# Performance work log

Hardware: AMD Instinct MI355X
Metric: run time of the kernel (lower is better)

## Reference

```python
import jax, jax.numpy as jnp
import numpy as np

N_NODES = 100000
N_EDGES = 1600000
IN_DIM, HID_DIM, OUT_DIM = 2, 128, 128


def setup_inputs() -> dict:
    key = jax.random.key(0)
    ks = jax.random.split(key, 8)
    x = jax.random.normal(ks[0], (N_NODES, IN_DIM), dtype=jnp.float32)
    edge_index = jax.random.randint(ks[1], (2, N_EDGES), 0, N_NODES, dtype=jnp.int64)
    s = 0.1
    return {
        "x": x,
        "edge_index": edge_index,
        # SAGEConv layer 1: lin_l (on aggregated neighbors, with bias) + lin_r (root)
        "W_l1": jax.random.normal(ks[2], (IN_DIM, HID_DIM), dtype=jnp.float32) * s,
        "W_r1": jax.random.normal(ks[3], (IN_DIM, HID_DIM), dtype=jnp.float32) * s,
        "b1": jnp.zeros((HID_DIM,), dtype=jnp.float32),
        # SAGEConv layer 2
        "W_l2": jax.random.normal(ks[4], (HID_DIM, OUT_DIM), dtype=jnp.float32) * s,
        "W_r2": jax.random.normal(ks[5], (HID_DIM, OUT_DIM), dtype=jnp.float32) * s,
        "b2": jnp.zeros((OUT_DIM,), dtype=jnp.float32),
    }


def _sage_conv(h, src, dst, Wl, Wr, b):
    # PyG SAGEConv (aggr='mean'): out_i = Wl @ mean_{j in N(i)} h_j + Wr @ h_i + b
    msg = h[src]                                              # [E, D] gather
    agg = jax.ops.segment_sum(msg, dst, num_segments=N_NODES)  # [N, D] scatter-add
    deg = jax.ops.segment_sum(jnp.ones_like(dst, dtype=h.dtype), dst,
                              num_segments=N_NODES)
    agg = agg / jnp.maximum(deg, 1.0)[:, None]                # mean aggregation
    return agg @ Wl + h @ Wr + b


def reference(x, edge_index, W_l1, W_r1, b1, W_l2, W_r2, b2):
    src, dst = edge_index[0], edge_index[1]  # messages flow src -> dst
    h = _sage_conv(x, src, dst, W_l1, W_r1, b1)
    h = jax.nn.relu(h)  # dropout p=0.1 is identity in eval mode
    out = _sage_conv(h, src, dst, W_l2, W_r2, b2)
    return out
```

## Files before the change

kernel.cpp:

```cpp
#include <hip/hip_runtime.h>


using f32x4 = __attribute__((ext_vector_type(4))) float;
using f32x2 = __attribute__((ext_vector_type(2))) float;
using s16x8 = __attribute__((ext_vector_type(8))) short;

__device__ __forceinline__ unsigned short f32_to_bf16(float f) {
  unsigned int u = __float_as_uint(f);
  u += 0x7fffu + ((u >> 16) & 1u);
  return (unsigned short)(u >> 16);
}

#define EDGE_TILE 4096

__global__ __launch_bounds__(256) void k_bhist(const int* __restrict__ ei, int* __restrict__ bcnt,
                                               unsigned short* __restrict__ hcnt, int E, int nb) {
  __shared__ int h[1024];
  int t = threadIdx.x;
  for (int i = t; i < nb; i += 256) h[i] = 0;
  __syncthreads();
  int tbeg = blockIdx.x * EDGE_TILE;
  int tend = min(tbeg + EDGE_TILE, E);
  const int* dstp = ei + E;
  for (int i = tbeg + t; i < tend; i += 256) atomicAdd(&h[dstp[i] >> 7], 1);
  __syncthreads();
  unsigned short* hr = hcnt + (size_t)blockIdx.x * nb;
  for (int i = t; i < nb; i += 256) {
    int c = h[i];
    hr[i] = (unsigned short)c;
    if (c) atomicAdd(&bcnt[i], c);
  }
}

__global__ __launch_bounds__(1024) void k_bscan(const int* __restrict__ bcnt, int* __restrict__ bbase,
                                                int nb, int E) {
  __shared__ int sm[2][1024];
  int t = threadIdx.x;
  int v0 = (t < nb) ? bcnt[t] : 0;
  sm[0][t] = v0;
  __syncthreads();
  int src = 0;
  for (int st = 1; st < 1024; st <<= 1) {
    int v = sm[src][t];
    if (t >= st) v += sm[src][t - st];
    sm[src ^ 1][t] = v; __syncthreads(); src ^= 1;
  }
  if (t < nb) bbase[t] = sm[src][t] - v0;
  if (t == 0) bbase[nb] = E;
}

__global__ __launch_bounds__(256) void k_colscan(const unsigned short* __restrict__ hcnt,
                                                 unsigned short* __restrict__ rel,
                                                 int nblk, int nb) {
  __shared__ int sm[2][256];
  int b = blockIdx.x;
  int t = threadIdx.x;
  int e0 = 2 * t, e1 = 2 * t + 1;
  int a = (e0 < nblk) ? (int)hcnt[(size_t)e0 * nb + b] : 0;
  int c = (e1 < nblk) ? (int)hcnt[(size_t)e1 * nb + b] : 0;
  int s = a + c;
  sm[0][t] = s;
  __syncthreads();
  int src = 0;
  for (int st = 1; st < 256; st <<= 1) {
    int v = sm[src][t];
    if (t >= st) v += sm[src][t - st];
    sm[src ^ 1][t] = v; __syncthreads(); src ^= 1;
  }
  int excl = sm[src][t] - s;
  if (e0 < nblk) rel[(size_t)e0 * nb + b] = (unsigned short)excl;
  if (e1 < nblk) rel[(size_t)e1 * nb + b] = (unsigned short)(excl + a);
}

__global__ __launch_bounds__(256) void k_bscatter(const int* __restrict__ ei,
                                                  const int* __restrict__ bbase,
                                                  const unsigned short* __restrict__ rel,
                                                  unsigned int* __restrict__ ebuf, int E, int nb) {
  __shared__ int h[1024];
  __shared__ int base[1024];
  int t = threadIdx.x;
  const unsigned short* rr = rel + (size_t)blockIdx.x * nb;
  for (int i = t; i < nb; i += 256) {
    h[i] = 0;
    base[i] = bbase[i] + (int)rr[i];
  }
  __syncthreads();
  int tbeg = blockIdx.x * EDGE_TILE;
  int tend = min(tbeg + EDGE_TILE, E);
  const int* srcp = ei;
  const int* dstp = ei + E;
  for (int i = tbeg + t; i < tend; i += 256) {
    int d = dstp[i];
    int b = d >> 7;
    int r = atomicAdd(&h[b], 1);
    ebuf[base[b] + r] = ((unsigned)srcp[i] << 7) | (unsigned)(d & 127);
  }
}

__global__ __launch_bounds__(256) void k_bucket_csr(const unsigned int* __restrict__ ebuf,
                                                    const int* __restrict__ bbase,
                                                    const float* __restrict__ x,
                                                    int* __restrict__ offs, int* __restrict__ csr,
                                                    float* __restrict__ agg1,
                                                    int N, int nb) {
  __shared__ int deg[128];
  __shared__ int loff[128];
  __shared__ int cur[128];
  __shared__ float sx0[128];
  __shared__ float sx1[128];
  int b = blockIdx.x;
  int t = threadIdx.x;
  int lo = bbase[b], hi = bbase[b + 1];
  if (t < 128) { deg[t] = 0; sx0[t] = 0.f; sx1[t] = 0.f; }
  __syncthreads();
  const float2* x2 = (const float2*)x;
  for (int i = lo + t; i < hi; i += 256) {
    unsigned int e = ebuf[i];
    int d = e & 127;
    float2 v = x2[e >> 7];
    atomicAdd(&deg[d], 1);
    atomicAdd(&sx0[d], v.x);
    atomicAdd(&sx1[d], v.y);
  }
  __syncthreads();
  if (t < 128) loff[t] = deg[t];
  __syncthreads();
  for (int st = 1; st < 128; st <<= 1) {
    int v = 0;
    if (t < 128 && t >= st) v = loff[t - st];
    __syncthreads();
    if (t < 128) loff[t] += v;
    __syncthreads();
  }
  if (t < 128) {
    int ex = loff[t] - deg[t];
    cur[t] = ex;
    int node = b * 128 + t;
    if (node < N) {
      offs[node] = lo + ex;
      agg1[2 * node]     = sx0[t];
      agg1[2 * node + 1] = sx1[t];
    }
  }
  if (b == nb - 1 && t == 0) offs[N] = hi;
  __syncthreads();
  for (int i = lo + t; i < hi; i += 256) {
    unsigned int e = ebuf[i];
    int r = atomicAdd(&cur[e & 127], 1);
    csr[lo + r] = (int)(e >> 7);
  }
}

__global__ __launch_bounds__(256) void k_layer1(const float* __restrict__ x, const float* __restrict__ agg1,
                                                const int* __restrict__ offs,
                                                const float* __restrict__ Wl, const float* __restrict__ Wr,
                                                const float* __restrict__ b1,
                                                unsigned int* __restrict__ h16,
                                                unsigned short* __restrict__ h8, int n) {
  int gid = blockIdx.x * 256 + threadIdx.x;
  int node = gid >> 6;
  if (node >= n) return;
  int c = (gid & 63) * 2;
  int deg = offs[node + 1] - offs[node];
  float sc = 1.0f / (float)max(deg, 1);
  float a0 = agg1[2 * node] * sc, a1 = agg1[2 * node + 1] * sc;
  float x0 = x[2 * node], x1 = x[2 * node + 1];
  float r0 = fmaf(a0, Wl[c],     fmaf(a1, Wl[128 + c],     fmaf(x0, Wr[c],     fmaf(x1, Wr[128 + c],     b1[c]))));
  float r1 = fmaf(a0, Wl[c + 1], fmaf(a1, Wl[128 + c + 1], fmaf(x0, Wr[c + 1], fmaf(x1, Wr[128 + c + 1], b1[c + 1]))));
  r0 = r0 > 0.f ? r0 : 0.f;
  r1 = r1 > 0.f ? r1 : 0.f;
  unsigned int packed = (unsigned int)f32_to_bf16(r0) | ((unsigned int)f32_to_bf16(r1) << 16);
  h16[(size_t)node * 64 + (gid & 63)] = packed;
  unsigned int p8 = (unsigned int)__builtin_amdgcn_cvt_pk_fp8_f32(r0, r1, 0, false);
  h8[(size_t)node * 64 + (gid & 63)] = (unsigned short)(p8 & 0xffffu);
}

__global__ __launch_bounds__(256) void k_prepw(const float* __restrict__ Wl2, const float* __restrict__ Wr2,
                                               unsigned short* __restrict__ wt) {
  int tid = blockIdx.x * 256 + threadIdx.x;
  if (tid >= 128 * 256) return;
  int c = tid >> 8, k = tid & 255;
  float v = (k < 128) ? Wl2[k * 128 + c] : Wr2[(k - 128) * 128 + c];
  wt[tid] = f32_to_bf16(v);
}

#define ACC8(v)                                                                              \
  do {                                                                                       \
    f32x2 p;                                                                                 \
    p = __builtin_amdgcn_cvt_pk_f32_fp8((int)(v).x, false); acc[0] += p[0];  acc[1] += p[1]; \
    p = __builtin_amdgcn_cvt_pk_f32_fp8((int)(v).x, true);  acc[2] += p[0];  acc[3] += p[1]; \
    p = __builtin_amdgcn_cvt_pk_f32_fp8((int)(v).y, false); acc[4] += p[0];  acc[5] += p[1]; \
    p = __builtin_amdgcn_cvt_pk_f32_fp8((int)(v).y, true);  acc[6] += p[0];  acc[7] += p[1]; \
    p = __builtin_amdgcn_cvt_pk_f32_fp8((int)(v).z, false); acc[8] += p[0];  acc[9] += p[1]; \
    p = __builtin_amdgcn_cvt_pk_f32_fp8((int)(v).z, true);  acc[10] += p[0]; acc[11] += p[1];\
    p = __builtin_amdgcn_cvt_pk_f32_fp8((int)(v).w, false); acc[12] += p[0]; acc[13] += p[1];\
    p = __builtin_amdgcn_cvt_pk_f32_fp8((int)(v).w, true);  acc[14] += p[0]; acc[15] += p[1];\
  } while (0)

__global__ __launch_bounds__(256) void k_agg2(const int* __restrict__ offs, const int* __restrict__ csr,
                                              const unsigned char* __restrict__ h8,
                                              unsigned int* __restrict__ a16, int n) {
  int wv   = threadIdx.x >> 6;
  int lane = threadIdx.x & 63;
  int sub  = lane >> 3;
  int cb   = lane & 7;
  int node = blockIdx.x * 32 + wv * 8 + sub;
  if (node >= n) return;
  int beg = offs[node];
  int end = offs[node + 1];
  int deg = end - beg;
  const unsigned char* hb = h8 + cb * 16;

  float acc[16];
#pragma unroll
  for (int j = 0; j < 16; ++j) acc[j] = 0.f;

  int t = 0;
  for (; t + 1 < deg; t += 2) {
    int s0 = csr[beg + t];
    int s1 = csr[beg + t + 1];
    uint4 v0 = *(const uint4*)(hb + (size_t)s0 * 128);
    uint4 v1 = *(const uint4*)(hb + (size_t)s1 * 128);
    ACC8(v0);
    ACC8(v1);
  }
  if (t < deg) {
    int s0 = csr[beg + t];
    uint4 v0 = *(const uint4*)(hb + (size_t)s0 * 128);
    ACC8(v0);
  }

  float scale = 1.0f / (float)max(deg, 1);
  unsigned int u[8];
#pragma unroll
  for (int k = 0; k < 8; ++k)
    u[k] = (unsigned int)f32_to_bf16(acc[2 * k] * scale) |
           ((unsigned int)f32_to_bf16(acc[2 * k + 1] * scale) << 16);
  unsigned int* dst = a16 + (size_t)node * 64 + cb * 8;
  *(uint4*)dst       = make_uint4(u[0], u[1], u[2], u[3]);
  *(uint4*)(dst + 4) = make_uint4(u[4], u[5], u[6], u[7]);
}

__global__ __launch_bounds__(256) void k_gemm(const unsigned short* __restrict__ a16,
                                              const unsigned short* __restrict__ h16,
                                              const unsigned short* __restrict__ wt,
                                              const float* __restrict__ b2,
                                              float* __restrict__ out, int nrows) {
  __shared__ unsigned short bs[64 * 264];
  int half = blockIdx.x & 1;
  int tg   = blockIdx.x >> 1;

#pragma unroll
  for (int i = 0; i < 8; ++i) {
    int c = threadIdx.x + i * 256;
    int row = c >> 5, off = c & 31;
    *(uint4*)(bs + row * 264 + off * 8) =
        *(const uint4*)(wt + ((size_t)(half * 64 + row)) * 256 + off * 8);
  }
  __syncthreads();

  int wv   = threadIdx.x >> 6;
  int lane = threadIdx.x & 63;
  int m16 = lane & 15, quad = lane >> 4;
  int tile = tg * 4 + wv;
  if (tile * 16 >= nrows) return;

  int r  = tile * 16 + m16;
  int rc = r < nrows ? r : nrows - 1;
  const unsigned short* arow = a16 + (size_t)rc * 128 + quad * 8;
  const unsigned short* hrow = h16 + (size_t)rc * 128 + quad * 8;

  s16x8 afrag[8];
#pragma unroll
  for (int c4 = 0; c4 < 4; ++c4) {
    afrag[c4]     = *(const s16x8*)(arow + c4 * 32);
    afrag[4 + c4] = *(const s16x8*)(hrow + c4 * 32);
  }

  f32x4 acc[4];
#pragma unroll
  for (int t = 0; t < 4; ++t) acc[t] = (f32x4){0.f, 0.f, 0.f, 0.f};

  const unsigned short* bbase = bs + m16 * 264 + quad * 8;
#pragma unroll
  for (int ch = 0; ch < 8; ++ch) {
#pragma unroll
    for (int t = 0; t < 4; ++t) {
      s16x8 bf = *(const s16x8*)(bbase + t * 16 * 264 + ch * 32);
      acc[t] = __builtin_amdgcn_mfma_f32_16x16x32_bf16(afrag[ch], bf, acc[t], 0, 0, 0);
    }
  }

#pragma unroll
  for (int t = 0; t < 4; ++t) {
    int col = half * 64 + t * 16 + m16;
    float bias = b2[col];
#pragma unroll
    for (int i = 0; i < 4; ++i) {
      int row = tile * 16 + quad * 4 + i;
      if (row < nrows) out[(size_t)row * 128 + col] = acc[t][i] + bias;
    }
  }
}

extern "C" void kernel_launch(void* const* d_in, const int* in_sizes, int n_in,
                              void* d_out, int out_size, void* d_ws, size_t ws_size,
                              hipStream_t stream) {
  const float* x    = (const float*)d_in[0];
  const int*   ei   = (const int*)d_in[1];
  const float* Wl1  = (const float*)d_in[2];
  const float* Wr1  = (const float*)d_in[3];
  const float* b1   = (const float*)d_in[4];
  const float* Wl2  = (const float*)d_in[5];
  const float* Wr2  = (const float*)d_in[6];
  const float* b2   = (const float*)d_in[7];
  float* out = (float*)d_out;

  const int N = in_sizes[0] / 2;
  const int E = in_sizes[1] / 2;
  const int nb = (N + 127) >> 7;
  const int nblk_e = (E + EDGE_TILE - 1) / EDGE_TILE;

  char* p = (char*)d_ws;
  auto take = [&](size_t bytes) { char* r = p; p += (bytes + 255) & ~(size_t)255; return r; };
  int* bcnt            = (int*)take(1024 * 4);
  int* bbase           = (int*)take(1025 * 4);
  unsigned short* hcnt = (unsigned short*)take((size_t)nblk_e * nb * 2);
  unsigned short* rel  = (unsigned short*)take((size_t)nblk_e * nb * 2);
  int* offs            = (int*)take((size_t)(N + 1) * 4);
  int* csr             = (int*)take((size_t)E * 4);
  unsigned int* ebuf   = (unsigned int*)take((size_t)E * 4);
  float* agg1          = (float*)take((size_t)N * 2 * 4);
  unsigned short* h16  = (unsigned short*)take((size_t)N * 128 * 2);
  unsigned short* a16  = (unsigned short*)take((size_t)N * 128 * 2);
  unsigned short* h8   = (unsigned short*)take((size_t)N * 128);
  unsigned short* wt   = (unsigned short*)take((size_t)128 * 256 * 2);

  const int ntiles = (N + 15) / 16;

  hipMemsetAsync(bcnt, 0, 1024 * 4, stream);

  k_bhist     <<<nblk_e, 256, 0, stream>>>(ei, bcnt, hcnt, E, nb);
  k_bscan     <<<1, 1024, 0, stream>>>(bcnt, bbase, nb, E);
  k_colscan   <<<nb, 256, 0, stream>>>(hcnt, rel, nblk_e, nb);
  k_bscatter  <<<nblk_e, 256, 0, stream>>>(ei, bbase, rel, ebuf, E, nb);
  k_bucket_csr<<<nb, 256, 0, stream>>>(ebuf, bbase, x, offs, csr, agg1, N, nb);
  k_layer1    <<<((size_t)N * 64 + 255) / 256, 256, 0, stream>>>(x, agg1, offs, Wl1, Wr1, b1,
                                                                 (unsigned int*)h16, h8, N);
  k_prepw     <<<(128 * 256) / 256, 256, 0, stream>>>(Wl2, Wr2, wt);
  k_agg2      <<<(N + 31) / 32, 256, 0, stream>>>(offs, csr, (const unsigned char*)h8,
                                                  (unsigned int*)a16, N);
  k_gemm      <<<((ntiles + 3) / 4) * 2, 256, 0, stream>>>(a16, h16, wt, b2, out, N);
}
```

Measured before the change: 246.3 us.

## Fuse layer-2 neighbor aggregation and GEMM into one kernel via LDS

Merges the fp8 gather-mean aggregation kernel with the bf16 MFMA GEMM. Each 32-node block aggregates into shared memory, then four waves each compute a 16x64 output tile from that. This drops the global round trip of the aggregated bf16 matrix and one kernel launch. Weight tiles are now read straight from global/L2 instead of being staged in LDS, and the GEMM phase waits on the slowest node's aggregation in each block.

```diff
diff --git a/kernel.cpp b/kernel.cpp
--- a/kernel.cpp
+++ b/kernel.cpp
@@ -197,108 +197,100 @@
     p = __builtin_amdgcn_cvt_pk_f32_fp8((int)(v).w, true);  acc[14] += p[0]; acc[15] += p[1];\
   } while (0)
 
-__global__ __launch_bounds__(256) void k_agg2(const int* __restrict__ offs, const int* __restrict__ csr,
-                                              const unsigned char* __restrict__ h8,
-                                              unsigned int* __restrict__ a16, int n) {
+__global__ __launch_bounds__(256) void k_aggemm(const int* __restrict__ offs, const int* __restrict__ csr,
+                                                const unsigned char* __restrict__ h8,
+                                                const unsigned short* __restrict__ h16,
+                                                const unsigned short* __restrict__ wt,
+                                                const float* __restrict__ b2,
+                                                float* __restrict__ out, int n) {
+  __shared__ unsigned short lds_a[32 * 136];
   int wv   = threadIdx.x >> 6;
   int lane = threadIdx.x & 63;
-  int sub  = lane >> 3;
-  int cb   = lane & 7;
-  int node = blockIdx.x * 32 + wv * 8 + sub;
-  if (node >= n) return;
-  int beg = offs[node];
-  int end = offs[node + 1];
-  int deg = end - beg;
-  const unsigned char* hb = h8 + cb * 16;
-
-  float acc[16];
-#pragma unroll
-  for (int j = 0; j < 16; ++j) acc[j] = 0.f;
-
-  int t = 0;
-  for (; t + 1 < deg; t += 2) {
-    int s0 = csr[beg + t];
-    int s1 = csr[beg + t + 1];
-    uint4 v0 = *(const uint4*)(hb + (size_t)s0 * 128);
-    uint4 v1 = *(const uint4*)(hb + (size_t)s1 * 128);
-    ACC8(v0);
-    ACC8(v1);
-  }
-  if (t < deg) {
-    int s0 = csr[beg + t];
-    uint4 v0 = *(const uint4*)(hb + (size_t)s0 * 128);
-    ACC8(v0);
-  }
-
-  float scale = 1.0f / (float)max(deg, 1);
-  unsigned int u[8];
-#pragma unroll
-  for (int k = 0; k < 8; ++k)
-    u[k] = (unsigned int)f32_to_bf16(acc[2 * k] * scale) |
-           ((unsigned int)f32_to_bf16(acc[2 * k + 1] * scale) << 16);
-  unsigned int* dst = a16 + (size_t)node * 64 + cb * 8;
-  *(uint4*)dst       = make_uint4(u[0], u[1], u[2], u[3]);
-  *(uint4*)(dst + 4) = make_uint4(u[4], u[5], u[6], u[7]);
-}
-
-__global__ __launch_bounds__(256) void k_gemm(const unsigned short* __restrict__ a16,
-                                              const unsigned short* __restrict__ h16,
-                                              const unsigned short* __restrict__ wt,
-                                              const float* __restrict__ b2,
-                                              float* __restrict__ out, int nrows) {
-  __shared__ unsigned short bs[64 * 264];
-  int half = blockIdx.x & 1;
-  int tg   = blockIdx.x >> 1;
-
-#pragma unroll
-  for (int i = 0; i < 8; ++i) {
-    int c = threadIdx.x + i * 256;
-    int row = c >> 5, off = c & 31;
-    *(uint4*)(bs + row * 264 + off * 8) =
-        *(const uint4*)(wt + ((size_t)(half * 64 + row)) * 256 + off * 8);
-  }
-  __syncthreads();
-
-  int wv   = threadIdx.x >> 6;
-  int lane = threadIdx.x & 63;
-  int m16 = lane & 15, quad = lane >> 4;
-  int tile = tg * 4 + wv;
-  if (tile * 16 >= nrows) return;
-
-  int r  = tile * 16 + m16;
-  int rc = r < nrows ? r : nrows - 1;
-  const unsigned short* arow = a16 + (size_t)rc * 128 + quad * 8;
-  const unsigned short* hrow = h16 + (size_t)rc * 128 + quad * 8;
-
-  s16x8 afrag[8];
-#pragma unroll
-  for (int c4 = 0; c4 < 4; ++c4) {
-    afrag[c4]     = *(const s16x8*)(arow + c4 * 32);
-    afrag[4 + c4] = *(const s16x8*)(hrow + c4 * 32);
-  }
-
-  f32x4 acc[4];
-#pragma unroll
-  for (int t = 0; t < 4; ++t) acc[t] = (f32x4){0.f, 0.f, 0.f, 0.f};
-
-  const unsigned short* bbase = bs + m16 * 264 + quad * 8;
-#pragma unroll
-  for (int ch = 0; ch < 8; ++ch) {
+
+  {
+    int sub  = lane >> 3;
+    int cb   = lane & 7;
+    int nr   = wv * 8 + sub;
+    int node = blockIdx.x * 32 + nr;
+
+    float acc[16];
+#pragma unroll
+    for (int j = 0; j < 16; ++j) acc[j] = 0.f;
+    int deg = 1;
+
+    if (node < n) {
+      int beg = offs[node];
+      int end = offs[node + 1];
+      deg = end - beg;
+      const unsigned char* hb = h8 + cb * 16;
+      int t = 0;
+      for (; t + 1 < deg; t += 2) {
+        int s0 = csr[beg + t];
+        int s1 = csr[beg + t + 1];
+        uint4 v0 = *(const uint4*)(hb + (size_t)s0 * 128);
+        uint4 v1 = *(const uint4*)(hb + (size_t)s1 * 128);
+        ACC8(v0);
+        ACC8(v1);
+      }
+      if (t < deg) {
+        int s0 = csr[beg + t];
+        uint4 v0 = *(const uint4*)(hb + (size_t)s0 * 128);
+        ACC8(v0);
+      }
+    }
+
+    float scale = 1.0f / (float)max(deg, 1);
+    unsigned int u[8];
+#pragma unroll
+    for (int k = 0; k < 8; ++k)
+      u[k] = (unsigned int)f32_to_bf16(acc[2 * k] * scale) |
+             ((unsigned int)f32_to_bf16(acc[2 * k + 1] * scale) << 16);
+    unsigned short* dstl = lds_a + nr * 136 + cb * 16;
+    *(uint4*)dstl       = make_uint4(u[0], u[1], u[2], u[3]);
+    *(uint4*)(dstl + 8) = make_uint4(u[4], u[5], u[6], u[7]);
+  }
+  __syncthreads();
+
+  {
+    int rowbase = (wv >> 1) * 16;
+    int colbase = (wv & 1) * 64;
+    int m16 = lane & 15, quad = lane >> 4;
+
+    int r  = blockIdx.x * 32 + rowbase + m16;
+    int rc = r < n ? r : n - 1;
+    const unsigned short* hrow = h16 + (size_t)rc * 128 + quad * 8;
+    const unsigned short* alds = lds_a + (rowbase + m16) * 136 + quad * 8;
+
+    s16x8 afrag[8];
+#pragma unroll
+    for (int c4 = 0; c4 < 4; ++c4) {
+      afrag[c4]     = *(const s16x8*)(alds + c4 * 32);
+      afrag[4 + c4] = *(const s16x8*)(hrow + c4 * 32);
+    }
+
+    f32x4 acc[4];
+#pragma unroll
+    for (int t = 0; t < 4; ++t) acc[t] = (f32x4){0.f, 0.f, 0.f, 0.f};
+
+    const unsigned short* bbase = wt + (size_t)(colbase + m16) * 256 + quad * 8;
+#pragma unroll
+    for (int ch = 0; ch < 8; ++ch) {
+#pragma unroll
+      for (int t = 0; t < 4; ++t) {
+        s16x8 bf = *(const s16x8*)(bbase + (size_t)t * 16 * 256 + ch * 32);
+        acc[t] = __builtin_amdgcn_mfma_f32_16x16x32_bf16(afrag[ch], bf, acc[t], 0, 0, 0);
+      }
+    }
+
 #pragma unroll
     for (int t = 0; t < 4; ++t) {
-      s16x8 bf = *(const s16x8*)(bbase + t * 16 * 264 + ch * 32);
-      acc[t] = __builtin_amdgcn_mfma_f32_16x16x32_bf16(afrag[ch], bf, acc[t], 0, 0, 0);
-    }
-  }
-
-#pragma unroll
-  for (int t = 0; t < 4; ++t) {
-    int col = half * 64 + t * 16 + m16;
-    float bias = b2[col];
-#pragma unroll
-    for (int i = 0; i < 4; ++i) {
-      int row = tile * 16 + quad * 4 + i;
-      if (row < nrows) out[(size_t)row * 128 + col] = acc[t][i] + bias;
+      int col = colbase + t * 16 + m16;
+      float bias = b2[col];
+#pragma unroll
+      for (int i = 0; i < 4; ++i) {
+        int row = blockIdx.x * 32 + rowbase + quad * 4 + i;
+        if (row < n) out[(size_t)row * 128 + col] = acc[t][i] + bias;
+      }
     }
   }
 }
@@ -332,11 +324,8 @@
   unsigned int* ebuf   = (unsigned int*)take((size_t)E * 4);
   float* agg1          = (float*)take((size_t)N * 2 * 4);
   unsigned short* h16  = (unsigned short*)take((size_t)N * 128 * 2);
-  unsigned short* a16  = (unsigned short*)take((size_t)N * 128 * 2);
   unsigned short* h8   = (unsigned short*)take((size_t)N * 128);
   unsigned short* wt   = (unsigned short*)take((size_t)128 * 256 * 2);
-
-  const int ntiles = (N + 15) / 16;
 
   hipMemsetAsync(bcnt, 0, 1024 * 4, stream);
 
@@ -348,7 +337,6 @@
   k_layer1    <<<((size_t)N * 64 + 255) / 256, 256, 0, stream>>>(x, agg1, offs, Wl1, Wr1, b1,
                                                                  (unsigned int*)h16, h8, N);
   k_prepw     <<<(128 * 256) / 256, 256, 0, stream>>>(Wl2, Wr2, wt);
-  k_agg2      <<<(N + 31) / 32, 256, 0, stream>>>(offs, csr, (const unsigned char*)h8,
-                                                  (unsigned int*)a16, N);
-  k_gemm      <<<((ntiles + 3) / 4) * 2, 256, 0, stream>>>(a16, h16, wt, b2, out, N);
-}
+  k_aggemm    <<<(N + 31) / 32, 256, 0, stream>>>(offs, csr, (const unsigned char*)h8,
+                                                  h16, wt, b2, out, N);
+}
```

Result: slower. 278.4 us (+13.0%).

## Fuse scans and weight prep into one launch, fold layer1 into bucket CSR

Applied to the files above, without the earlier changes.

Merges the bucket-base scan, the per-bucket column scan and the layer-2 weight transpose into a single multi-role kernel. Layer-1 compute now runs inside the bucket CSR kernel using the shared-memory degree and aggregate sums, which removes the agg1 round trip and two launches. The agg2 gather loop is software-pipelined so the next pair of neighbour rows is loaded before the current pair is accumulated. The cost is a longer tail in the bucket kernel, which runs only about 782 blocks, and higher register pressure in agg2.

```diff
diff --git a/kernel.cpp b/kernel.cpp
--- a/kernel.cpp
+++ b/kernel.cpp
@@ -32,44 +32,64 @@
   }
 }
 
-__global__ __launch_bounds__(1024) void k_bscan(const int* __restrict__ bcnt, int* __restrict__ bbase,
-                                                int nb, int E) {
-  __shared__ int sm[2][1024];
+__global__ __launch_bounds__(256) void k_scans(const unsigned short* __restrict__ hcnt,
+                                               unsigned short* __restrict__ rel,
+                                               const int* __restrict__ bcnt,
+                                               int* __restrict__ bbase,
+                                               const float* __restrict__ Wl2,
+                                               const float* __restrict__ Wr2,
+                                               unsigned short* __restrict__ wt,
+                                               int nblk, int nb, int E) {
+  __shared__ int sm[2][256];
+  int bb = blockIdx.x;
   int t = threadIdx.x;
-  int v0 = (t < nb) ? bcnt[t] : 0;
-  sm[0][t] = v0;
-  __syncthreads();
-  int src = 0;
-  for (int st = 1; st < 1024; st <<= 1) {
-    int v = sm[src][t];
-    if (t >= st) v += sm[src][t - st];
-    sm[src ^ 1][t] = v; __syncthreads(); src ^= 1;
-  }
-  if (t < nb) bbase[t] = sm[src][t] - v0;
-  if (t == 0) bbase[nb] = E;
-}
-
-__global__ __launch_bounds__(256) void k_colscan(const unsigned short* __restrict__ hcnt,
-                                                 unsigned short* __restrict__ rel,
-                                                 int nblk, int nb) {
-  __shared__ int sm[2][256];
-  int b = blockIdx.x;
-  int t = threadIdx.x;
-  int e0 = 2 * t, e1 = 2 * t + 1;
-  int a = (e0 < nblk) ? (int)hcnt[(size_t)e0 * nb + b] : 0;
-  int c = (e1 < nblk) ? (int)hcnt[(size_t)e1 * nb + b] : 0;
-  int s = a + c;
-  sm[0][t] = s;
-  __syncthreads();
-  int src = 0;
-  for (int st = 1; st < 256; st <<= 1) {
-    int v = sm[src][t];
-    if (t >= st) v += sm[src][t - st];
-    sm[src ^ 1][t] = v; __syncthreads(); src ^= 1;
-  }
-  int excl = sm[src][t] - s;
-  if (e0 < nblk) rel[(size_t)e0 * nb + b] = (unsigned short)excl;
-  if (e1 < nblk) rel[(size_t)e1 * nb + b] = (unsigned short)(excl + a);
+
+  if (bb < nb) {
+    int b = bb;
+    int e0 = 2 * t, e1 = 2 * t + 1;
+    int a = (e0 < nblk) ? (int)hcnt[(size_t)e0 * nb + b] : 0;
+    int c = (e1 < nblk) ? (int)hcnt[(size_t)e1 * nb + b] : 0;
+    int s = a + c;
+    sm[0][t] = s;
+    __syncthreads();
+    int src = 0;
+    for (int st = 1; st < 256; st <<= 1) {
+      int v = sm[src][t];
+      if (t >= st) v += sm[src][t - st];
+      sm[src ^ 1][t] = v; __syncthreads(); src ^= 1;
+    }
+    int excl = sm[src][t] - s;
+    if (e0 < nblk) rel[(size_t)e0 * nb + b] = (unsigned short)excl;
+    if (e1 < nblk) rel[(size_t)e1 * nb + b] = (unsigned short)(excl + a);
+  } else if (bb == nb) {
+    int i0 = t * 4;
+    int v0 = (i0     < nb) ? bcnt[i0]     : 0;
+    int v1 = (i0 + 1 < nb) ? bcnt[i0 + 1] : 0;
+    int v2 = (i0 + 2 < nb) ? bcnt[i0 + 2] : 0;
+    int v3 = (i0 + 3 < nb) ? bcnt[i0 + 3] : 0;
+    int s = v0 + v1 + v2 + v3;
+    sm[0][t] = s;
+    __syncthreads();
+    int src = 0;
+    for (int st = 1; st < 256; st <<= 1) {
+      int v = sm[src][t];
+      if (t >= st) v += sm[src][t - st];
+      sm[src ^ 1][t] = v; __syncthreads(); src ^= 1;
+    }
+    int ex = sm[src][t] - s;
+    if (i0     < nb) bbase[i0]     = ex; ex += v0;
+    if (i0 + 1 < nb) bbase[i0 + 1] = ex; ex += v1;
+    if (i0 + 2 < nb) bbase[i0 + 2] = ex; ex += v2;
+    if (i0 + 3 < nb) bbase[i0 + 3] = ex;
+    if (t == 255) bbase[nb] = E;
+  } else {
+    int tid = (bb - nb - 1) * 256 + t;
+    if (tid < 128 * 256) {
+      int c = tid >> 8, k = tid & 255;
+      float v = (k < 128) ? Wl2[k * 128 + c] : Wr2[(k - 128) * 128 + c];
+      wt[tid] = f32_to_bf16(v);
+    }
+  }
 }
 
 __global__ __launch_bounds__(256) void k_bscatter(const int* __restrict__ ei,
@@ -100,8 +120,12 @@
 __global__ __launch_bounds__(256) void k_bucket_csr(const unsigned int* __restrict__ ebuf,
                                                     const int* __restrict__ bbase,
                                                     const float* __restrict__ x,
+                                                    const float* __restrict__ Wl,
+                                                    const float* __restrict__ Wr,
+                                                    const float* __restrict__ b1,
                                                     int* __restrict__ offs, int* __restrict__ csr,
-                                                    float* __restrict__ agg1,
+                                                    unsigned int* __restrict__ h16,
+                                                    unsigned short* __restrict__ h8,
                                                     int N, int nb) {
   __shared__ int deg[128];
   __shared__ int loff[128];
@@ -136,11 +160,7 @@
     int ex = loff[t] - deg[t];
     cur[t] = ex;
     int node = b * 128 + t;
-    if (node < N) {
-      offs[node] = lo + ex;
-      agg1[2 * node]     = sx0[t];
-      agg1[2 * node + 1] = sx1[t];
-    }
+    if (node < N) offs[node] = lo + ex;
   }
   if (b == nb - 1 && t == 0) offs[N] = hi;
   __syncthreads();
@@ -149,39 +169,26 @@
     int r = atomicAdd(&cur[e & 127], 1);
     csr[lo + r] = (int)(e >> 7);
   }
-}
-
-__global__ __launch_bounds__(256) void k_layer1(const float* __restrict__ x, const float* __restrict__ agg1,
-                                                const int* __restrict__ offs,
-                                                const float* __restrict__ Wl, const float* __restrict__ Wr,
-                                                const float* __restrict__ b1,
-                                                unsigned int* __restrict__ h16,
-                                                unsigned short* __restrict__ h8, int n) {
-  int gid = blockIdx.x * 256 + threadIdx.x;
-  int node = gid >> 6;
-  if (node >= n) return;
-  int c = (gid & 63) * 2;
-  int deg = offs[node + 1] - offs[node];
-  float sc = 1.0f / (float)max(deg, 1);
-  float a0 = agg1[2 * node] * sc, a1 = agg1[2 * node + 1] * sc;
-  float x0 = x[2 * node], x1 = x[2 * node + 1];
-  float r0 = fmaf(a0, Wl[c],     fmaf(a1, Wl[128 + c],     fmaf(x0, Wr[c],     fmaf(x1, Wr[128 + c],     b1[c]))));
-  float r1 = fmaf(a0, Wl[c + 1], fmaf(a1, Wl[128 + c + 1], fmaf(x0, Wr[c + 1], fmaf(x1, Wr[128 + c + 1], b1[c + 1]))));
-  r0 = r0 > 0.f ? r0 : 0.f;
-  r1 = r1 > 0.f ? r1 : 0.f;
-  unsigned int packed = (unsigned int)f32_to_bf16(r0) | ((unsigned int)f32_to_bf16(r1) << 16);
-  h16[(size_t)node * 64 + (gid & 63)] = packed;
-  unsigned int p8 = (unsigned int)__builtin_amdgcn_cvt_pk_fp8_f32(r0, r1, 0, false);
-  h8[(size_t)node * 64 + (gid & 63)] = (unsigned short)(p8 & 0xffffu);
-}
-
-__global__ __launch_bounds__(256) void k_prepw(const float* __restrict__ Wl2, const float* __restrict__ Wr2,
-                                               unsigned short* __restrict__ wt) {
-  int tid = blockIdx.x * 256 + threadIdx.x;
-  if (tid >= 128 * 256) return;
-  int c = tid >> 8, k = tid & 255;
-  float v = (k < 128) ? Wl2[k * 128 + c] : Wr2[(k - 128) * 128 + c];
-  wt[tid] = f32_to_bf16(v);
+
+  int nfirst = b * 128;
+  for (int i = t; i < 128 * 64; i += 256) {
+    int nl = i >> 6;
+    int node = nfirst + nl;
+    if (node >= N) break;
+    int c = (i & 63) * 2;
+    int dg = deg[nl];
+    float sc = 1.0f / (float)max(dg, 1);
+    float a0 = sx0[nl] * sc, a1 = sx1[nl] * sc;
+    float2 xv = x2[node];
+    float r0 = fmaf(a0, Wl[c],     fmaf(a1, Wl[128 + c],     fmaf(xv.x, Wr[c],     fmaf(xv.y, Wr[128 + c],     b1[c]))));
+    float r1 = fmaf(a0, Wl[c + 1], fmaf(a1, Wl[128 + c + 1], fmaf(xv.x, Wr[c + 1], fmaf(xv.y, Wr[128 + c + 1], b1[c + 1]))));
+    r0 = r0 > 0.f ? r0 : 0.f;
+    r1 = r1 > 0.f ? r1 : 0.f;
+    unsigned int packed = (unsigned int)f32_to_bf16(r0) | ((unsigned int)f32_to_bf16(r1) << 16);
+    h16[(size_t)node * 64 + (i & 63)] = packed;
+    unsigned int p8 = (unsigned int)__builtin_amdgcn_cvt_pk_fp8_f32(r0, r1, 0, false);
+    h8[(size_t)node * 64 + (i & 63)] = (unsigned short)(p8 & 0xffffu);
+  }
 }
 
 #define ACC8(v)                                                                              \
@@ -216,13 +223,22 @@
   for (int j = 0; j < 16; ++j) acc[j] = 0.f;
 
   int t = 0;
-  for (; t + 1 < deg; t += 2) {
-    int s0 = csr[beg + t];
-    int s1 = csr[beg + t + 1];
-    uint4 v0 = *(const uint4*)(hb + (size_t)s0 * 128);
-    uint4 v1 = *(const uint4*)(hb + (size_t)s1 * 128);
-    ACC8(v0);
-    ACC8(v1);
+  if (deg >= 2) {
+    int s0 = csr[beg];
+    int s1 = csr[beg + 1];
+    uint4 c0 = *(const uint4*)(hb + (size_t)s0 * 128);
+    uint4 c1 = *(const uint4*)(hb + (size_t)s1 * 128);
+    for (t = 2; t + 1 < deg; t += 2) {
+      int n0 = csr[beg + t];
+      int n1 = csr[beg + t + 1];
+      uint4 p0 = *(const uint4*)(hb + (size_t)n0 * 128);
+      uint4 p1 = *(const uint4*)(hb + (size_t)n1 * 128);
+      ACC8(c0);
+      ACC8(c1);
+      c0 = p0; c1 = p1;
+    }
+    ACC8(c0);
+    ACC8(c1);
   }
   if (t < deg) {
     int s0 = csr[beg + t];
@@ -330,7 +346,6 @@
   int* offs            = (int*)take((size_t)(N + 1) * 4);
   int* csr             = (int*)take((size_t)E * 4);
   unsigned int* ebuf   = (unsigned int*)take((size_t)E * 4);
-  float* agg1          = (float*)take((size_t)N * 2 * 4);
   unsigned short* h16  = (unsigned short*)take((size_t)N * 128 * 2);
   unsigned short* a16  = (unsigned short*)take((size_t)N * 128 * 2);
   unsigned short* h8   = (unsigned short*)take((size_t)N * 128);
@@ -341,13 +356,11 @@
   hipMemsetAsync(bcnt, 0, 1024 * 4, stream);
 
   k_bhist     <<<nblk_e, 256, 0, stream>>>(ei, bcnt, hcnt, E, nb);
-  k_bscan     <<<1, 1024, 0, stream>>>(bcnt, bbase, nb, E);
-  k_colscan   <<<nb, 256, 0, stream>>>(hcnt, rel, nblk_e, nb);
+  k_scans     <<<nb + 1 + 128, 256, 0, stream>>>(hcnt, rel, bcnt, bbase, Wl2, Wr2, wt,
+                                                 nblk_e, nb, E);
   k_bscatter  <<<nblk_e, 256, 0, stream>>>(ei, bbase, rel, ebuf, E, nb);
-  k_bucket_csr<<<nb, 256, 0, stream>>>(ebuf, bbase, x, offs, csr, agg1, N, nb);
-  k_layer1    <<<((size_t)N * 64 + 255) / 256, 256, 0, stream>>>(x, agg1, offs, Wl1, Wr1, b1,
-                                                                 (unsigned int*)h16, h8, N);
-  k_prepw     <<<(128 * 256) / 256, 256, 0, stream>>>(Wl2, Wr2, wt);
+  k_bucket_csr<<<nb, 256, 0, stream>>>(ebuf, bbase, x, Wl1, Wr1, b1, offs, csr,
+                                       (unsigned int*)h16, h8, N, nb);
   k_agg2      <<<(N + 31) / 32, 256, 0, stream>>>(offs, csr, (const unsigned char*)h8,
                                                   (unsigned int*)a16, N);
   k_gemm      <<<((ntiles + 3) / 4) * 2, 256, 0, stream>>>(a16, h16, wt, b2, out, N);
```

Result: no change. 242.0 us (-1.7%).
